# Optimization experiments

Measured on AMD Instinct MI355X. Metric: run time of the kernel, lower is better.

The kernel has to match this reference:

```python
import jax, jax.numpy as jnp
import numpy as np

CONTEXT = 256   # context_size
INITIAL = 32    # initial_size
HIDDEN = 256    # hidden_size
WINDOW = 64 - 1 # module stores window_size - 1
TEMP = 50000.0  # soft-argmax temperature
MAX_STEPS = CONTEXT - INITIAL  # cur_pt >= 1 guarantees >=1 index advance per step
B = 4096


def setup_inputs() -> dict:
    key = jax.random.key(0)
    ks = jax.random.split(key, 4)
    def lin_w(k, fan_in, fan_out):
        bound = 1.0 / np.sqrt(fan_in)
        return jax.random.uniform(k, (fan_in, fan_out), jnp.float32, -bound, bound)
    return {
        "x": jax.random.normal(ks[0], (B, CONTEXT), jnp.float32),
        "hid_W": lin_w(ks[1], HIDDEN, HIDDEN),
        "hid_b": jnp.zeros((HIDDEN,), jnp.float32),
        "in_W": lin_w(ks[2], INITIAL, HIDDEN),
        "in_b": jnp.zeros((HIDDEN,), jnp.float32),
        "pred_W": lin_w(ks[3], HIDDEN, WINDOW),
        "pred_b": jnp.zeros((WINDOW,), jnp.float32),
    }


def reference(x, hid_W, hid_b, in_W, in_b, pred_W, pred_b):
    # with per-item active masks. Padded/dense outputs:
    #   pts  [B, MAX_STEPS] : predicted change points (last point dropped, rest zero-padded)
    #   mx   [B, CONTEXT]   : all sigmoid-masked slices scattered back to their positions
    # returned concatenated as [B, MAX_STEPS + CONTEXT].
    Bv = x.shape[0]
    rows = jnp.arange(Bv)[:, None]
    jW = jnp.arange(WINDOW, dtype=jnp.float32)
    iI = jnp.arange(INITIAL)
    iWin = jnp.arange(WINDOW)

    def step(carry, _):
        last, hidden, masked_x, count = carry
        active = last < CONTEXT                       # torch: skip items whose last pt >= context
        last_long = last.astype(jnp.int32)            # floor (last >= INITIAL > 0)
        # slice x[i, last-INITIAL : last]; first step last=INITIAL -> x[:, 0:INITIAL]
        idx = last_long[:, None] - INITIAL + iI       # [B, I]
        slices = jnp.take_along_axis(x, idx, axis=1)
        new_hidden = jnp.tanh(hidden @ hid_W + hid_b + slices @ in_W + in_b)
        hidden = jnp.where(active[:, None], new_hidden, hidden)
        w = new_hidden @ pred_W + pred_b              # [B, WINDOW]
        p = jax.nn.softmax(w * TEMP, axis=-1)
        cur_pt = jnp.minimum(p @ jW + 1.0, float(WINDOW))        # soft-argmax + 1, clamped
        seq_end = jnp.minimum(cur_pt + last, float(CONTEXT))
        seq_end_long = seq_end.astype(jnp.int32)
        # masked slice: mask = 1 - sigmoid(j - cur_pt), j in [0, seq_end_long - last_long)
        pos = last_long[:, None] + iWin                            # [B, WINDOW]
        valid = (pos < seq_end_long[:, None]) & active[:, None]
        mask = 1.0 - jax.nn.sigmoid(jW[None, :] - cur_pt[:, None])
        pos_c = jnp.clip(pos, 0, CONTEXT - 1)
        xg = jnp.take_along_axis(x, pos_c, axis=1)
        contrib = jnp.where(valid, mask * xg, 0.0)
        masked_x = masked_x.at[rows, pos_c].add(contrib)           # segments are disjoint
        last = jnp.where(active, seq_end, last)
        count = count + active.astype(jnp.int32)
        return (last, hidden, masked_x, count), jnp.where(active, seq_end, 0.0)

    init = (jnp.full((Bv,), float(INITIAL), jnp.float32),
            jnp.ones((Bv, HIDDEN), jnp.float32),
            jnp.zeros_like(x),
            jnp.zeros((Bv,), jnp.int32))
    (last, hidden, masked_x, count), ys = jax.lax.scan(step, init, None, length=MAX_STEPS)
    pts = ys.T                                                    # [B, MAX_STEPS]
    keep = jnp.arange(MAX_STEPS)[None, :] < (count - 1)[:, None]  # torch drops last pt per item
    pts = jnp.where(keep, pts, 0.0)
    return jnp.concatenate([pts, masked_x], axis=1)               # [B, MAX_STEPS + CONTEXT]
```

## Files before the change

kernel.cpp:

```cpp
#include <hip/hip_runtime.h>
#include <math.h>


#define CTX     256
#define INIT    32
#define HID     256
#define WIN     63
#define MSTEPS  224
#define OUTROW  (MSTEPS + CTX)
#define IT      4
#define NT      256

__global__ void __launch_bounds__(NT)
cpp_kernel(const float* __restrict__ x,
           const float* __restrict__ hid_W,
           const float* __restrict__ hid_b,
           const float* __restrict__ in_W,
           const float* __restrict__ in_b,
           const float* __restrict__ pred_W,
           const float* __restrict__ pred_b,
           float* __restrict__ out)
{
    __shared__ float  s_x[IT][CTX];
    __shared__ float  s_hid[IT][HID];
    __shared__ double s_pred[IT][4][64];
    __shared__ float  s_last[IT];
    __shared__ int    s_lastl[IT];
    __shared__ int    s_act[IT];

    const int tid   = threadIdx.x;
    const int lane  = tid & 63;
    const int q     = tid >> 6;
    const int item0 = blockIdx.x * IT;

    #pragma unroll
    for (int it = 0; it < IT; ++it) {
        s_x[it][tid]   = x[(size_t)(item0 + it) * CTX + tid];
        s_hid[it][tid] = 1.0f;
    }
    for (int idx = tid; idx < IT * OUTROW; idx += NT)
        out[(size_t)item0 * OUTROW + idx] = 0.0f;
    if (tid < IT) { s_last[tid] = (float)INIT; s_lastl[tid] = INIT; s_act[tid] = 1; }
    __syncthreads();

    int sc = 0;

    for (int iter = 0; iter < MSTEPS; ++iter) {
        int lastl[IT], act[IT];
        #pragma unroll
        for (int it = 0; it < IT; ++it) { lastl[it] = s_lastl[it]; act[it] = s_act[it]; }
        if (!(act[0] | act[1] | act[2] | act[3])) break;

        const int j = tid;
        double acc[IT];
        {
            const double b = (double)hid_b[j] + (double)in_b[j];
            #pragma unroll
            for (int it = 0; it < IT; ++it) acc[it] = b;
        }

        int sb[IT];
        #pragma unroll
        for (int it = 0; it < IT; ++it)
            sb[it] = (lastl[it] < CTX ? lastl[it] : CTX) - INIT;

        #pragma unroll 4
        for (int m = 0; m < INIT; ++m) {
            const double wv = (double)in_W[m * HID + j];
            #pragma unroll
            for (int it = 0; it < IT; ++it)
                acc[it] = fma((double)s_x[it][sb[it] + m], wv, acc[it]);
        }

        for (int k = 0; k < HID; k += 4) {
            float hv[IT][4];
            #pragma unroll
            for (int it = 0; it < IT; ++it) {
                const float4 v = *(const float4*)&s_hid[it][k];
                hv[it][0] = v.x; hv[it][1] = v.y; hv[it][2] = v.z; hv[it][3] = v.w;
            }
            #pragma unroll
            for (int u = 0; u < 4; ++u) {
                const double wv = (double)hid_W[(size_t)(k + u) * HID + j];
                #pragma unroll
                for (int it = 0; it < IT; ++it)
                    acc[it] = fma((double)hv[it][u], wv, acc[it]);
            }
        }

        float nh[IT];
        #pragma unroll
        for (int it = 0; it < IT; ++it) nh[it] = tanhf((float)acc[it]);

        __syncthreads();
        #pragma unroll
        for (int it = 0; it < IT; ++it) if (act[it]) s_hid[it][j] = nh[it];
        __syncthreads();

        double pacc[IT] = {0.0, 0.0, 0.0, 0.0};
        if (lane < WIN) {
            const int k0 = q * 64;
            #pragma unroll 4
            for (int kk = 0; kk < 64; ++kk) {
                const int k = k0 + kk;
                const double wv = (double)pred_W[k * WIN + lane];
                #pragma unroll
                for (int it = 0; it < IT; ++it)
                    pacc[it] = fma((double)s_hid[it][k], wv, pacc[it]);
            }
        }
        #pragma unroll
        for (int it = 0; it < IT; ++it) s_pred[it][q][lane] = pacc[it];
        __syncthreads();

        {
            const int it = q;
            float t = -INFINITY;
            if (lane < WIN) {
                const double wv = s_pred[it][0][lane] + s_pred[it][1][lane]
                                + s_pred[it][2][lane] + s_pred[it][3][lane]
                                + (double)pred_b[lane];
                const float wf = (float)wv;
                t = wf * 50000.0f;
            }
            float mx = t;
            #pragma unroll
            for (int off = 32; off > 0; off >>= 1)
                mx = fmaxf(mx, __shfl_xor(mx, off));
            const float e = (lane < WIN) ? expf(t - mx) : 0.0f;
            float S = e;
            #pragma unroll
            for (int off = 32; off > 0; off >>= 1)
                S += __shfl_xor(S, off);
            const float p = e / S;
            float D = p * (float)lane;
            #pragma unroll
            for (int off = 32; off > 0; off >>= 1)
                D += __shfl_xor(D, off);
            float cur = D + 1.0f;
            cur = fminf(cur, 63.0f);
            const float lastf = s_last[it];
            float se = cur + lastf;
            se = fminf(se, 256.0f);
            const int sel = (int)se;

            if (act[it]) {
                float* orow = out + (size_t)(item0 + it) * OUTROW;
                if (lane < WIN) {
                    const int pos = lastl[it] + lane;
                    if (pos < sel) {
                        const float msk = 1.0f / (1.0f + expf((float)lane - cur));
                        orow[MSTEPS + pos] = msk * s_x[it][pos];
                    }
                }
                if (lane == 0) {
                    if (se < 256.0f) orow[sc] = se;
                    s_last[it]  = se;
                    s_lastl[it] = sel;
                    s_act[it]   = (se < 256.0f) ? 1 : 0;
                }
                sc++;
            }
        }
        __syncthreads();
    }
}

extern "C" void kernel_launch(void* const* d_in, const int* in_sizes, int n_in,
                              void* d_out, int out_size, void* d_ws, size_t ws_size,
                              hipStream_t stream) {
    const float* x      = (const float*)d_in[0];
    const float* hid_W  = (const float*)d_in[1];
    const float* hid_b  = (const float*)d_in[2];
    const float* in_W   = (const float*)d_in[3];
    const float* in_b   = (const float*)d_in[4];
    const float* pred_W = (const float*)d_in[5];
    const float* pred_b = (const float*)d_in[6];
    float* out = (float*)d_out;

    const int B = in_sizes[0] / CTX;
    const int nblocks = B / IT;
    cpp_kernel<<<nblocks, NT, 0, stream>>>(x, hid_W, hid_b, in_W, in_b,
                                           pred_W, pred_b, out);
}
```

Baseline: 379.4 us.

## Double threads per block and split hidden matvec K across two halves

Raises the block size from 256 to 512 threads and splits the hidden-state matvec's K dimension unevenly. One half handles the input projection plus K[0,112), the other handles K[112,256), and the partial sums are combined through shared memory before tanh. The prediction matvec is likewise split over 8 waves with an 8-way reduction. Shared x and hidden state are now stored as doubles, which removes float-to-double conversions in the inner loops. In exchange it adds a barrier per step and doubles the shared footprint, which may reduce occupancy.

```diff
diff --git a/kernel.cpp b/kernel.cpp
--- a/kernel.cpp
+++ b/kernel.cpp
@@ -9,7 +9,8 @@
 #define MSTEPS  224
 #define OUTROW  (MSTEPS + CTX)
 #define IT      4
-#define NT      256
+#define NT      512
+#define KSPLIT  112
 
 __global__ void __launch_bounds__(NT)
 cpp_kernel(const float* __restrict__ x,
@@ -21,9 +22,9 @@
            const float* __restrict__ pred_b,
            float* __restrict__ out)
 {
-    __shared__ float  s_x[IT][CTX];
-    __shared__ float  s_hid[IT][HID];
-    __shared__ double s_pred[IT][4][64];
+    __shared__ double s_x[IT][CTX];
+    __shared__ double s_hid[IT][HID];
+    __shared__ double s_scr[IT][8][64];
     __shared__ float  s_last[IT];
     __shared__ int    s_lastl[IT];
     __shared__ int    s_act[IT];
@@ -31,16 +32,21 @@
     const int tid   = threadIdx.x;
     const int lane  = tid & 63;
     const int q     = tid >> 6;
+    const int j     = tid & (HID - 1);
+    const int half  = tid >> 8;
     const int item0 = blockIdx.x * IT;
 
-    #pragma unroll
-    for (int it = 0; it < IT; ++it) {
-        s_x[it][tid]   = x[(size_t)(item0 + it) * CTX + tid];
-        s_hid[it][tid] = 1.0f;
-    }
+    for (int idx = tid; idx < IT * CTX; idx += NT)
+        s_x[idx >> 8][idx & 255] = (double)x[(size_t)(item0 + (idx >> 8)) * CTX + (idx & 255)];
+    for (int idx = tid; idx < IT * HID; idx += NT)
+        s_hid[idx >> 8][idx & 255] = 1.0;
     for (int idx = tid; idx < IT * OUTROW; idx += NT)
         out[(size_t)item0 * OUTROW + idx] = 0.0f;
     if (tid < IT) { s_last[tid] = (float)INIT; s_lastl[tid] = INIT; s_act[tid] = 1; }
+
+    const double bias = (half == 0) ? ((double)hid_b[j] + (double)in_b[j]) : 0.0;
+    double* const red = &s_scr[0][0][0];
+
     __syncthreads();
 
     int sc = 0;
@@ -51,77 +57,92 @@
         for (int it = 0; it < IT; ++it) { lastl[it] = s_lastl[it]; act[it] = s_act[it]; }
         if (!(act[0] | act[1] | act[2] | act[3])) break;
 
-        const int j = tid;
         double acc[IT];
+        #pragma unroll
+        for (int it = 0; it < IT; ++it) acc[it] = bias;
+
+        if (half == 0) {
+            int sb[IT];
+            #pragma unroll
+            for (int it = 0; it < IT; ++it) sb[it] = lastl[it] - INIT;
+            #pragma unroll 4
+            for (int m = 0; m < INIT; ++m) {
+                const double wv = (double)in_W[m * HID + j];
+                #pragma unroll
+                for (int it = 0; it < IT; ++it)
+                    acc[it] = fma(s_x[it][sb[it] + m], wv, acc[it]);
+            }
+        }
+
         {
-            const double b = (double)hid_b[j] + (double)in_b[j];
-            #pragma unroll
-            for (int it = 0; it < IT; ++it) acc[it] = b;
-        }
-
-        int sb[IT];
-        #pragma unroll
-        for (int it = 0; it < IT; ++it)
-            sb[it] = (lastl[it] < CTX ? lastl[it] : CTX) - INIT;
-
-        #pragma unroll 4
-        for (int m = 0; m < INIT; ++m) {
-            const double wv = (double)in_W[m * HID + j];
+            const int kbeg = (half == 0) ? 0 : KSPLIT;
+            const int kend = (half == 0) ? KSPLIT : HID;
+            for (int k = kbeg; k < kend; k += 4) {
+                double2 hA[IT], hB[IT];
+                #pragma unroll
+                for (int it = 0; it < IT; ++it) {
+                    hA[it] = *(const double2*)&s_hid[it][k];
+                    hB[it] = *(const double2*)&s_hid[it][k + 2];
+                }
+                const double w0 = (double)hid_W[(size_t)(k + 0) * HID + j];
+                const double w1 = (double)hid_W[(size_t)(k + 1) * HID + j];
+                const double w2 = (double)hid_W[(size_t)(k + 2) * HID + j];
+                const double w3 = (double)hid_W[(size_t)(k + 3) * HID + j];
+                #pragma unroll
+                for (int it = 0; it < IT; ++it) {
+                    acc[it] = fma(hA[it].x, w0, acc[it]);
+                    acc[it] = fma(hA[it].y, w1, acc[it]);
+                    acc[it] = fma(hB[it].x, w2, acc[it]);
+                    acc[it] = fma(hB[it].y, w3, acc[it]);
+                }
+            }
+        }
+
+        if (half == 1) {
+            #pragma unroll
+            for (int it = 0; it < IT; ++it) red[it * HID + j] = acc[it];
+        }
+        __syncthreads();
+
+        if (half == 0) {
+            float nh[IT];
+            #pragma unroll
+            for (int it = 0; it < IT; ++it) {
+                acc[it] += red[it * HID + j];
+                nh[it] = tanhf((float)acc[it]);
+            }
             #pragma unroll
             for (int it = 0; it < IT; ++it)
-                acc[it] = fma((double)s_x[it][sb[it] + m], wv, acc[it]);
-        }
-
-        for (int k = 0; k < HID; k += 4) {
-            float hv[IT][4];
-            #pragma unroll
-            for (int it = 0; it < IT; ++it) {
-                const float4 v = *(const float4*)&s_hid[it][k];
-                hv[it][0] = v.x; hv[it][1] = v.y; hv[it][2] = v.z; hv[it][3] = v.w;
-            }
-            #pragma unroll
-            for (int u = 0; u < 4; ++u) {
-                const double wv = (double)hid_W[(size_t)(k + u) * HID + j];
-                #pragma unroll
-                for (int it = 0; it < IT; ++it)
-                    acc[it] = fma((double)hv[it][u], wv, acc[it]);
-            }
-        }
-
-        float nh[IT];
-        #pragma unroll
-        for (int it = 0; it < IT; ++it) nh[it] = tanhf((float)acc[it]);
-
-        __syncthreads();
-        #pragma unroll
-        for (int it = 0; it < IT; ++it) if (act[it]) s_hid[it][j] = nh[it];
+                if (act[it]) s_hid[it][j] = (double)nh[it];
+        }
         __syncthreads();
 
         double pacc[IT] = {0.0, 0.0, 0.0, 0.0};
         if (lane < WIN) {
-            const int k0 = q * 64;
+            const int kb = q * 32;
             #pragma unroll 4
-            for (int kk = 0; kk < 64; ++kk) {
-                const int k = k0 + kk;
+            for (int kk = 0; kk < 32; ++kk) {
+                const int k = kb + kk;
                 const double wv = (double)pred_W[k * WIN + lane];
                 #pragma unroll
                 for (int it = 0; it < IT; ++it)
-                    pacc[it] = fma((double)s_hid[it][k], wv, pacc[it]);
+                    pacc[it] = fma(s_hid[it][k], wv, pacc[it]);
             }
         }
         #pragma unroll
-        for (int it = 0; it < IT; ++it) s_pred[it][q][lane] = pacc[it];
-        __syncthreads();
-
-        {
+        for (int it = 0; it < IT; ++it) s_scr[it][q][lane] = pacc[it];
+        __syncthreads();
+
+        if (q < IT) {
             const int it = q;
             float t = -INFINITY;
             if (lane < WIN) {
-                const double wv = s_pred[it][0][lane] + s_pred[it][1][lane]
-                                + s_pred[it][2][lane] + s_pred[it][3][lane]
+                const double wv = s_scr[it][0][lane] + s_scr[it][1][lane]
+                                + s_scr[it][2][lane] + s_scr[it][3][lane]
+                                + s_scr[it][4][lane] + s_scr[it][5][lane]
+                                + s_scr[it][6][lane] + s_scr[it][7][lane]
                                 + (double)pred_b[lane];
-                const float wf = (float)wv;
-                t = wf * 50000.0f;
+                t = (float)wv * 50000.0f;
             }
             float mx = t;
             #pragma unroll
@@ -139,8 +160,7 @@
                 D += __shfl_xor(D, off);
             float cur = D + 1.0f;
             cur = fminf(cur, 63.0f);
-            const float lastf = s_last[it];
-            float se = cur + lastf;
+            float se = cur + s_last[it];
             se = fminf(se, 256.0f);
             const int sel = (int)se;
 
@@ -150,7 +170,7 @@
                     const int pos = lastl[it] + lane;
                     if (pos < sel) {
                         const float msk = 1.0f / (1.0f + expf((float)lane - cur));
-                        orow[MSTEPS + pos] = msk * s_x[it][pos];
+                        orow[MSTEPS + pos] = msk * (float)s_x[it][pos];
                     }
                 }
                 if (lane == 0) {
```

New measurement: 328.9 us. 1.15x faster.

## Store state as double in LDS and give each wave a full per-item prediction matvec

Applied to the files above, without the earlier changes.

The input row and hidden state are now kept as double in shared memory, which removes the per-FMA float-to-double conversions in the recurrent and input matvecs. The prediction projection no longer splits K across the four waves and reduces partials through shared memory. Each wave now computes its own item's full 256-long dot product, which drops the s_pred buffer and one block barrier per step and skips finished items. In exchange, each lane loads pred_W four times as often, shared-memory footprint and bandwidth for the state double, and `last` is carried in a register.

```diff
diff --git a/kernel.cpp b/kernel.cpp
--- a/kernel.cpp
+++ b/kernel.cpp
@@ -21,29 +21,35 @@
            const float* __restrict__ pred_b,
            float* __restrict__ out)
 {
-    __shared__ float  s_x[IT][CTX];
-    __shared__ float  s_hid[IT][HID];
-    __shared__ double s_pred[IT][4][64];
-    __shared__ float  s_last[IT];
+    __shared__ double s_x[IT][CTX];
+    __shared__ double s_hid[IT][HID];
     __shared__ int    s_lastl[IT];
     __shared__ int    s_act[IT];
 
-    const int tid   = threadIdx.x;
-    const int lane  = tid & 63;
-    const int q     = tid >> 6;
+    const int tid  = threadIdx.x;
+    const int lane = tid & 63;
+    const int q    = tid >> 6;
+    const int j    = tid;
     const int item0 = blockIdx.x * IT;
 
-    #pragma unroll
-    for (int it = 0; it < IT; ++it) {
-        s_x[it][tid]   = x[(size_t)(item0 + it) * CTX + tid];
-        s_hid[it][tid] = 1.0f;
+    const double bias  = (double)hid_b[j] + (double)in_b[j];
+    const float  pbias = (lane < WIN) ? pred_b[lane] : 0.0f;
+
+    {
+        const int item = item0 + q;
+        float* orow = out + (size_t)item * OUTROW;
+        for (int idx = lane; idx < OUTROW; idx += 64) orow[idx] = 0.0f;
+        #pragma unroll
+        for (int u = 0; u < 4; ++u)
+            s_x[q][lane + 64 * u] = (double)x[(size_t)item * CTX + lane + 64 * u];
+        #pragma unroll
+        for (int u = 0; u < 4; ++u) s_hid[q][lane + 64 * u] = 1.0;
+        if (lane == 0) { s_lastl[q] = INIT; s_act[q] = 1; }
     }
-    for (int idx = tid; idx < IT * OUTROW; idx += NT)
-        out[(size_t)item0 * OUTROW + idx] = 0.0f;
-    if (tid < IT) { s_last[tid] = (float)INIT; s_lastl[tid] = INIT; s_act[tid] = 1; }
+
+    float mylast = (float)INIT;
+    int   sc = 0;
     __syncthreads();
-
-    int sc = 0;
 
     for (int iter = 0; iter < MSTEPS; ++iter) {
         int lastl[IT], act[IT];
@@ -51,77 +57,66 @@
         for (int it = 0; it < IT; ++it) { lastl[it] = s_lastl[it]; act[it] = s_act[it]; }
         if (!(act[0] | act[1] | act[2] | act[3])) break;
 
-        const int j = tid;
         double acc[IT];
+        #pragma unroll
+        for (int it = 0; it < IT; ++it) acc[it] = bias;
+
         {
-            const double b = (double)hid_b[j] + (double)in_b[j];
+            int sb[IT];
             #pragma unroll
-            for (int it = 0; it < IT; ++it) acc[it] = b;
+            for (int it = 0; it < IT; ++it) {
+                int l = lastl[it]; if (l > CTX) l = CTX;
+                sb[it] = l - INIT;
+            }
+            #pragma unroll 4
+            for (int m = 0; m < INIT; ++m) {
+                const double wv = (double)in_W[m * HID + j];
+                #pragma unroll
+                for (int it = 0; it < IT; ++it)
+                    acc[it] = fma(s_x[it][sb[it] + m], wv, acc[it]);
+            }
         }
+        for (int k = 0; k < HID; k += 4) {
+            const double w0 = (double)hid_W[(size_t)(k + 0) * HID + j];
+            const double w1 = (double)hid_W[(size_t)(k + 1) * HID + j];
+            const double w2 = (double)hid_W[(size_t)(k + 2) * HID + j];
+            const double w3 = (double)hid_W[(size_t)(k + 3) * HID + j];
+            #pragma unroll
+            for (int it = 0; it < IT; ++it) {
+                const double2 hA = *(const double2*)&s_hid[it][k];
+                const double2 hB = *(const double2*)&s_hid[it][k + 2];
+                acc[it] = fma(hA.x, w0, acc[it]);
+                acc[it] = fma(hA.y, w1, acc[it]);
+                acc[it] = fma(hB.x, w2, acc[it]);
+                acc[it] = fma(hB.y, w3, acc[it]);
+            }
+        }
+        __syncthreads();
 
-        int sb[IT];
         #pragma unroll
         for (int it = 0; it < IT; ++it)
-            sb[it] = (lastl[it] < CTX ? lastl[it] : CTX) - INIT;
-
-        #pragma unroll 4
-        for (int m = 0; m < INIT; ++m) {
-            const double wv = (double)in_W[m * HID + j];
-            #pragma unroll
-            for (int it = 0; it < IT; ++it)
-                acc[it] = fma((double)s_x[it][sb[it] + m], wv, acc[it]);
-        }
-
-        for (int k = 0; k < HID; k += 4) {
-            float hv[IT][4];
-            #pragma unroll
-            for (int it = 0; it < IT; ++it) {
-                const float4 v = *(const float4*)&s_hid[it][k];
-                hv[it][0] = v.x; hv[it][1] = v.y; hv[it][2] = v.z; hv[it][3] = v.w;
-            }
-            #pragma unroll
-            for (int u = 0; u < 4; ++u) {
-                const double wv = (double)hid_W[(size_t)(k + u) * HID + j];
-                #pragma unroll
-                for (int it = 0; it < IT; ++it)
-                    acc[it] = fma((double)hv[it][u], wv, acc[it]);
-            }
-        }
-
-        float nh[IT];
-        #pragma unroll
-        for (int it = 0; it < IT; ++it) nh[it] = tanhf((float)acc[it]);
-
-        __syncthreads();
-        #pragma unroll
-        for (int it = 0; it < IT; ++it) if (act[it]) s_hid[it][j] = nh[it];
+            if (act[it]) s_hid[it][j] = (double)tanhf((float)acc[it]);
         __syncthreads();
 
-        double pacc[IT] = {0.0, 0.0, 0.0, 0.0};
-        if (lane < WIN) {
-            const int k0 = q * 64;
-            #pragma unroll 4
-            for (int kk = 0; kk < 64; ++kk) {
-                const int k = k0 + kk;
-                const double wv = (double)pred_W[k * WIN + lane];
-                #pragma unroll
-                for (int it = 0; it < IT; ++it)
-                    pacc[it] = fma((double)s_hid[it][k], wv, pacc[it]);
-            }
-        }
-        #pragma unroll
-        for (int it = 0; it < IT; ++it) s_pred[it][q][lane] = pacc[it];
-        __syncthreads();
-
-        {
+        if (act[q]) {
             const int it = q;
             float t = -INFINITY;
             if (lane < WIN) {
-                const double wv = s_pred[it][0][lane] + s_pred[it][1][lane]
-                                + s_pred[it][2][lane] + s_pred[it][3][lane]
-                                + (double)pred_b[lane];
-                const float wf = (float)wv;
-                t = wf * 50000.0f;
+                double wacc = 0.0;
+                for (int k = 0; k < HID; k += 4) {
+                    const double p0 = (double)pred_W[(k + 0) * WIN + lane];
+                    const double p1 = (double)pred_W[(k + 1) * WIN + lane];
+                    const double p2 = (double)pred_W[(k + 2) * WIN + lane];
+                    const double p3 = (double)pred_W[(k + 3) * WIN + lane];
+                    const double2 hA = *(const double2*)&s_hid[it][k];
+                    const double2 hB = *(const double2*)&s_hid[it][k + 2];
+                    wacc = fma(hA.x, p0, wacc);
+                    wacc = fma(hA.y, p1, wacc);
+                    wacc = fma(hB.x, p2, wacc);
+                    wacc = fma(hB.y, p3, wacc);
+                }
+                const double wv = wacc + (double)pbias;
+                t = (float)wv * 50000.0f;
             }
             float mx = t;
             #pragma unroll
@@ -137,30 +132,25 @@
             #pragma unroll
             for (int off = 32; off > 0; off >>= 1)
                 D += __shfl_xor(D, off);
-            float cur = D + 1.0f;
-            cur = fminf(cur, 63.0f);
-            const float lastf = s_last[it];
-            float se = cur + lastf;
-            se = fminf(se, 256.0f);
+            float cur = fminf(D + 1.0f, 63.0f);
+            float se = fminf(cur + mylast, 256.0f);
             const int sel = (int)se;
 
-            if (act[it]) {
-                float* orow = out + (size_t)(item0 + it) * OUTROW;
-                if (lane < WIN) {
-                    const int pos = lastl[it] + lane;
-                    if (pos < sel) {
-                        const float msk = 1.0f / (1.0f + expf((float)lane - cur));
-                        orow[MSTEPS + pos] = msk * s_x[it][pos];
-                    }
+            float* orow = out + (size_t)(item0 + it) * OUTROW;
+            if (lane < WIN) {
+                const int pos = lastl[it] + lane;
+                if (pos < sel) {
+                    const float msk = 1.0f / (1.0f + expf((float)lane - cur));
+                    orow[MSTEPS + pos] = msk * (float)s_x[it][pos];
                 }
-                if (lane == 0) {
-                    if (se < 256.0f) orow[sc] = se;
-                    s_last[it]  = se;
-                    s_lastl[it] = sel;
-                    s_act[it]   = (se < 256.0f) ? 1 : 0;
-                }
-                sc++;
             }
+            const bool done = (se >= 256.0f);
+            if (lane == 0) {
+                if (!done) { orow[sc] = se; s_lastl[it] = sel; }
+                else       { s_act[it] = 0; }
+            }
+            sc++;
+            mylast = se;
         }
         __syncthreads();
     }
```

Result: faster. 332.1 us (-12.5%).
